# Kernel optimization log

Hardware: AMD Instinct MI355X
Metric: run time of the kernel (lower is better)

Reference implementation:

```python
import jax, jax.numpy as jnp
import numpy as np
from jax import lax

B = 16384  # batch; original torch module runs unbatched (1,5,27), we vectorize over B


def _conv(x, w, b, ph):
    # NCHW conv with kernel (kh,1), padding (ph,0), stride 1
    y = lax.conv_general_dilated(x, w, (1, 1), [(ph, ph), (0, 0)],
                                 dimension_numbers=('NCHW', 'OIHW', 'NCHW'))
    return y + b[None, :, None, None]


def _sl(x, w, b):
    # Semi_Linear: shared Linear applied over every (channel, height) slice ->
    # algebraically a single batched matmul on the last axis. w: (out,in)
    return jnp.einsum('bchw,ow->bcho', x, w) + b


def setup_inputs() -> dict:
    key = jax.random.key(0)
    ks = iter(jax.random.split(key, 40))
    def p(shape):
        return jax.random.normal(next(ks), shape, jnp.float32) * 0.05
    d = dict(
        x=jax.random.normal(next(ks), (B, 1, 5, 27), jnp.float32),
        w0a=p((5, 1, 3, 1)), b0a=p((5,)),
        wl0=p((18, 27)), bl0=p((18,)),
        w0b=p((25, 5, 3, 1)), b0b=p((25,)),
        w0c=p((25, 1, 1, 1)), b0c=p((25,)),
        wr0=p((18, 27)), br0=p((18,)),
        w1=p((75, 25, 2, 1)), b1=p((75,)),
        wl1=p((10, 18)), bl1=p((10,)),
        w2=p((125, 75, 2, 1)), b2=p((125,)),
        wa=p((125, 25, 3, 1)), ba=p((125,)),
        wra=p((10, 18)), bra=p((10,)),
        w0=p((300, 125, 2, 1)), b0=p((300,)),
        wl2=p((5, 10)), bl2=p((5,)),
        w0b2=p((512, 300, 2, 1)), b0b2=p((512,)),
        w0c2=p((512, 125, 3, 1)), b0c2=p((512,)),
        wr02=p((5, 10)), br02=p((5,)),
    )
    return d


def reference(x, w0a, b0a, wl0, bl0, w0b, b0b, w0c, b0c, wr0, br0,
              w1, b1, wl1, bl1, w2, b2, wa, ba, wra, bra,
              w0, b0, wl2, bl2, w0b2, b0b2, w0c2, b0c2, wr02, br02):
    # stage 0
    z = _conv(x, w0a, b0a, 1)                      # (B,5,5,27)
    z = jax.nn.relu(_sl(z, wl0, bl0))              # (B,5,5,18)
    z = _conv(z, w0b, b0b, 1)                      # (B,25,5,18)
    y = _conv(_sl(x, wr0, br0), w0c, b0c, 0)       # (B,25,5,18)
    x1 = z + y
    # stage 1
    z = _conv(x1, w1, b1, 0)                       # (B,75,4,18)
    z = jax.nn.relu(_sl(z, wl1, bl1))              # (B,75,4,10)
    z = _conv(z, w2, b2, 0)                        # (B,125,3,10)
    y = _conv(_sl(x1, wra, bra), wa, ba, 0)        # (B,125,3,10)
    x2 = z + y
    # stage 2
    z = _conv(x2, w0, b0, 0)                       # (B,300,2,10)
    z = jax.nn.relu(_sl(z, wl2, bl2))              # (B,300,2,5)
    z = _conv(z, w0b2, b0b2, 0)                    # (B,512,1,5)
    y = _conv(_sl(x2, wr02, br02), w0c2, b0c2, 0)  # (B,512,1,5)
    return z + y
```

## Files before the change

kernel.cpp:

```cpp
#include <hip/hip_runtime.h>
#include <stdint.h>


#define WB2T_OFF 0
#define WC2T_OFF 307200
#define W0T_OFF  499200
#define W1T_OFF  574200
#define WAT_OFF  577950
#define W2T_OFF  587325
#define WT_TOTAL 606075

__global__ __launch_bounds__(256)
void transpose_w(const float* __restrict__ w1, const float* __restrict__ wa,
                 const float* __restrict__ w2, const float* __restrict__ w0,
                 const float* __restrict__ wb2, const float* __restrict__ wc2,
                 float* __restrict__ ws) {
  int i = blockIdx.x * 256 + threadIdx.x;
  if (i < 3750) {
    int co = i / 50, k = i % 50;
    ws[W1T_OFF + k*75 + co] = w1[i];
  } else if (i < 13125) {
    int j = i - 3750; int co = j / 75, k = j % 75;
    ws[WAT_OFF + k*125 + co] = wa[j];
  } else if (i < 31875) {
    int j = i - 13125; int co = j / 150, k = j % 150;
    ws[W2T_OFF + k*125 + co] = w2[j];
  } else if (i < 106875) {
    int j = i - 31875; int co = j / 250, k = j % 250;
    ws[W0T_OFF + k*300 + co] = w0[j];
  } else if (i < 414075) {
    int j = i - 106875; int co = j / 600, k = j % 600;
    ws[WB2T_OFF + k*512 + co] = wb2[j];
  } else if (i < 606075) {
    int j = i - 414075; int co = j / 375, k = j % 375;
    ws[WC2T_OFF + k*512 + co] = wc2[j];
  }
}

template<int N>
__device__ __forceinline__ void ldrow(float* r, const float* p) {
  #pragma unroll
  for (int i = 0; i < N/4; ++i) {
    float4 q = reinterpret_cast<const float4*>(p)[i];
    r[4*i+0] = q.x; r[4*i+1] = q.y; r[4*i+2] = q.z; r[4*i+3] = q.w;
  }
}
template<int N>
__device__ __forceinline__ void strow(float* p, const float* r) {
  #pragma unroll
  for (int i = 0; i < N/4; ++i) {
    float4 q; q.x = r[4*i+0]; q.y = r[4*i+1]; q.z = r[4*i+2]; q.w = r[4*i+3];
    reinterpret_cast<float4*>(p)[i] = q;
  }
}

#define POOL   10112
#define X1_O   0
#define SX_O   2500
#define Z0A_O  2640
#define Z0SL_O 4500
#define T90_O  5000
#define Z1S_O  4500
#define T2_O   8100
#define X2_O   0
#define T3_O   4500
#define Z2S_O  6500

__global__ __launch_bounds__(256, 2)
void fused_net(const float* __restrict__ xg,
  const float* __restrict__ w0a_, const float* __restrict__ b0a_,
  const float* __restrict__ wl0_, const float* __restrict__ bl0_,
  const float* __restrict__ w0b_, const float* __restrict__ b0b_,
  const float* __restrict__ w0c_, const float* __restrict__ b0c_,
  const float* __restrict__ wr0_, const float* __restrict__ br0_,
  const float* __restrict__ b1_,
  const float* __restrict__ wl1_, const float* __restrict__ bl1_,
  const float* __restrict__ b2_,
  const float* __restrict__ ba_,
  const float* __restrict__ wra_, const float* __restrict__ bra_,
  const float* __restrict__ b0_,
  const float* __restrict__ wl2_, const float* __restrict__ bl2_,
  const float* __restrict__ b0b2_,
  const float* __restrict__ b0c2_,
  const float* __restrict__ wr02_,const float* __restrict__ br02_,
  const float* __restrict__ w1t, const float* __restrict__ wat,
  const float* __restrict__ w2t, const float* __restrict__ w0t,
  const float* __restrict__ wb2t, const float* __restrict__ wc2t,
  float* __restrict__ outg, int Btot)
{
  __shared__ __align__(16) float S[2*POOL];
  const int tid = threadIdx.x;
  const int b0 = blockIdx.x * 2;

  for (int i = tid; i < 270; i += 256) {
    int samp = i / 135, j = i % 135;
    int h = j / 27, w = j % 27;
    float v = 0.f;
    if (b0 + samp < Btot) v = xg[(size_t)(b0 + samp) * 135 + j];
    S[samp*POOL + SX_O + h*28 + w] = v;
  }
  __syncthreads();

  if (tid < 50) {
    int samp = tid / 25, r = tid % 25, co = r / 5, h = r % 5;
    float* P = S + samp*POOL;
    float acc[28];
    float bias = b0a_[co];
    #pragma unroll
    for (int w = 0; w < 28; ++w) acc[w] = bias;
    #pragma unroll
    for (int dh = 0; dh < 3; ++dh) {
      int hi = h + dh - 1;
      if (hi >= 0 && hi < 5) {
        float wf = w0a_[co*3 + dh];
        float row[28]; ldrow<28>(row, P + SX_O + hi*28);
        #pragma unroll
        for (int w = 0; w < 27; ++w) acc[w] += row[w] * wf;
      }
    }
    strow<28>(P + Z0A_O + (co*5 + h)*28, acc);
  }
  __syncthreads();

  if (tid < 180) {
    int samp = tid / 90, r = tid % 90;
    float* P = S + samp*POOL;
    if (r < 75) {
      int c = r / 15, q = r % 15, h = q / 3, o0 = (q % 3) * 6;
      float row[28]; ldrow<28>(row, P + Z0A_O + (c*5 + h)*28);
      float acc[6];
      #pragma unroll
      for (int k = 0; k < 6; ++k) acc[k] = bl0_[o0 + k];
      for (int w = 0; w < 27; ++w) {
        float rv = row[w];
        #pragma unroll
        for (int k = 0; k < 6; ++k) acc[k] += rv * wl0_[(o0 + k)*27 + w];
      }
      float* dst = P + Z0SL_O + (c*5 + h)*20 + o0;
      #pragma unroll
      for (int k = 0; k < 6; ++k) dst[k] = fmaxf(acc[k], 0.f);
    } else {
      int q = r - 75, h = q / 3, o0 = (q % 3) * 6;
      float row[28]; ldrow<28>(row, P + SX_O + h*28);
      float acc[6];
      #pragma unroll
      for (int k = 0; k < 6; ++k) acc[k] = br0_[o0 + k];
      for (int w = 0; w < 27; ++w) {
        float rv = row[w];
        #pragma unroll
        for (int k = 0; k < 6; ++k) acc[k] += rv * wr0_[(o0 + k)*27 + w];
      }
      float* dst = P + T90_O + h*20 + o0;
      #pragma unroll
      for (int k = 0; k < 6; ++k) dst[k] = acc[k];
    }
  }
  __syncthreads();

  if (tid < 250) {
    int samp = tid / 125, r = tid % 125, co = r / 5, h = r % 5;
    float* P = S + samp*POOL;
    float tr[20]; ldrow<20>(tr, P + T90_O + h*20);
    float wc = w0c_[co];
    float base = b0b_[co] + b0c_[co];
    float acc[20];
    #pragma unroll
    for (int o = 0; o < 18; ++o) acc[o] = base + tr[o]*wc;
    acc[18] = 0.f; acc[19] = 0.f;
    #pragma unroll
    for (int dh = 0; dh < 3; ++dh) {
      int hi = h + dh - 1;
      if (hi >= 0 && hi < 5) {
        #pragma unroll
        for (int ci = 0; ci < 5; ++ci) {
          float wgt = w0b_[(co*5 + ci)*3 + dh];
          float row[20]; ldrow<20>(row, P + Z0SL_O + (ci*5 + hi)*20);
          #pragma unroll
          for (int o = 0; o < 18; ++o) acc[o] += row[o] * wgt;
        }
      }
    }
    strow<20>(P + X1_O + (co*5 + h)*20, acc);
  }
  __syncthreads();

  for (int t = tid; t < 850; t += 256) {
    if (t < 600) {
      int samp = t / 300, r = t % 300, co = r / 4, h = r % 4;
      float* P = S + samp*POOL;
      float z1[18];
      float bias = b1_[co];
      #pragma unroll
      for (int w = 0; w < 18; ++w) z1[w] = bias;
      for (int ci = 0; ci < 25; ++ci) {
        float wx = w1t[(ci*2 + 0)*75 + co];
        float wy = w1t[(ci*2 + 1)*75 + co];
        float r0[20], r1[20];
        ldrow<20>(r0, P + X1_O + (ci*5 + h    )*20);
        ldrow<20>(r1, P + X1_O + (ci*5 + h + 1)*20);
        #pragma unroll
        for (int w = 0; w < 18; ++w) z1[w] += r0[w]*wx + r1[w]*wy;
      }
      float out[12];
      #pragma unroll
      for (int o = 0; o < 10; ++o) {
        float acc = bl1_[o];
        #pragma unroll
        for (int w = 0; w < 18; ++w) acc += z1[w] * wl1_[o*18 + w];
        out[o] = fmaxf(acc, 0.f);
      }
      out[10] = 0.f; out[11] = 0.f;
      strow<12>(P + Z1S_O + (co*4 + h)*12, out);
    } else {
      int q = t - 600;
      int samp = q / 125, r = q % 125, c = r / 5, h = r % 5;
      float* P = S + samp*POOL;
      float row[20]; ldrow<20>(row, P + X1_O + (c*5 + h)*20);
      float out[12];
      #pragma unroll
      for (int o = 0; o < 10; ++o) {
        float acc = bra_[o];
        #pragma unroll
        for (int w = 0; w < 18; ++w) acc += row[w] * wra_[o*18 + w];
        out[o] = acc;
      }
      out[10] = 0.f; out[11] = 0.f;
      strow<12>(P + T2_O + (c*5 + h)*12, out);
    }
  }
  __syncthreads();

  if (tid < 250) {
    int samp = tid / 125, co = tid % 125;
    float* P = S + samp*POOL;
    float acc[3][10];
    float bias = b2_[co] + ba_[co];
    #pragma unroll
    for (int h = 0; h < 3; ++h)
      #pragma unroll
      for (int w = 0; w < 10; ++w) acc[h][w] = bias;
    for (int ci = 0; ci < 25; ++ci) {
      float wf0 = wat[(ci*3 + 0)*125 + co];
      float wf1 = wat[(ci*3 + 1)*125 + co];
      float wf2 = wat[(ci*3 + 2)*125 + co];
      float rr[5][12];
      #pragma unroll
      for (int hh = 0; hh < 5; ++hh) ldrow<12>(rr[hh], P + T2_O + (ci*5 + hh)*12);
      #pragma unroll
      for (int h = 0; h < 3; ++h)
        #pragma unroll
        for (int w = 0; w < 10; ++w)
          acc[h][w] += rr[h][w]*wf0 + rr[h+1][w]*wf1 + rr[h+2][w]*wf2;
    }
    #pragma unroll
    for (int h = 0; h < 3; ++h) {
      float out[12];
      #pragma unroll
      for (int w = 0; w < 10; ++w) out[w] = acc[h][w];
      out[10] = 0.f; out[11] = 0.f;
      strow<12>(P + X2_O + (co*3 + h)*12, out);
    }
  }
  __syncthreads();

  if (tid < 250) {
    int samp = tid / 125, co = tid % 125;
    float* P = S + samp*POOL;
    float acc[3][12];
    #pragma unroll
    for (int h = 0; h < 3; ++h) ldrow<12>(acc[h], P + X2_O + (co*3 + h)*12);
    for (int ci = 0; ci < 75; ++ci) {
      float wx = w2t[(ci*2 + 0)*125 + co];
      float wy = w2t[(ci*2 + 1)*125 + co];
      float rr[4][12];
      #pragma unroll
      for (int hh = 0; hh < 4; ++hh) ldrow<12>(rr[hh], P + Z1S_O + (ci*4 + hh)*12);
      #pragma unroll
      for (int h = 0; h < 3; ++h)
        #pragma unroll
        for (int w = 0; w < 10; ++w)
          acc[h][w] += rr[h][w]*wx + rr[h+1][w]*wy;
    }
    #pragma unroll
    for (int h = 0; h < 3; ++h) strow<12>(P + X2_O + (co*3 + h)*12, acc[h]);
  }
  __syncthreads();

  for (int t = tid; t < 400; t += 256) {
    if (t < 150) {
      int samp = t / 75, cot = t % 75;
      int co = cot * 4;
      float* P = S + samp*POOL;
      float acc[4][2][10];
      #pragma unroll
      for (int j = 0; j < 4; ++j) {
        float bb = b0_[co + j];
        #pragma unroll
        for (int h = 0; h < 2; ++h)
          #pragma unroll
          for (int w = 0; w < 10; ++w) acc[j][h][w] = bb;
      }
      for (int ci = 0; ci < 125; ++ci) {
        float a0[12], a1[12], a2[12];
        ldrow<12>(a0, P + X2_O + (ci*3 + 0)*12);
        ldrow<12>(a1, P + X2_O + (ci*3 + 1)*12);
        ldrow<12>(a2, P + X2_O + (ci*3 + 2)*12);
        float4 wxv = *reinterpret_cast<const float4*>(w0t + (ci*2 + 0)*300 + co);
        float4 wyv = *reinterpret_cast<const float4*>(w0t + (ci*2 + 1)*300 + co);
        float wx[4] = {wxv.x, wxv.y, wxv.z, wxv.w};
        float wy[4] = {wyv.x, wyv.y, wyv.z, wyv.w};
        #pragma unroll
        for (int j = 0; j < 4; ++j)
          #pragma unroll
          for (int w = 0; w < 10; ++w) {
            acc[j][0][w] += a0[w]*wx[j] + a1[w]*wy[j];
            acc[j][1][w] += a1[w]*wx[j] + a2[w]*wy[j];
          }
      }
      #pragma unroll
      for (int j = 0; j < 4; ++j) {
        float out[12];
        #pragma unroll
        for (int h = 0; h < 2; ++h)
          #pragma unroll
          for (int o = 0; o < 5; ++o) {
            float sacc = bl2_[o];
            #pragma unroll
            for (int w = 0; w < 10; ++w) sacc += acc[j][h][w] * wl2_[o*10 + w];
            out[h*5 + o] = fmaxf(sacc, 0.f);
          }
        out[10] = 0.f; out[11] = 0.f;
        strow<12>(P + Z2S_O + (co + j)*12, out);
      }
    } else {
      int q = t - 150;
      int samp = q / 125, c = q % 125;
      float* P = S + samp*POOL;
      float rr[3][12];
      #pragma unroll
      for (int h = 0; h < 3; ++h) ldrow<12>(rr[h], P + X2_O + (c*3 + h)*12);
      float out[16];
      #pragma unroll
      for (int h = 0; h < 3; ++h)
        #pragma unroll
        for (int o = 0; o < 5; ++o) {
          float acc = br02_[o];
          #pragma unroll
          for (int w = 0; w < 10; ++w) acc += rr[h][w] * wr02_[o*10 + w];
          out[h*5 + o] = acc;
        }
      out[15] = 0.f;
      strow<16>(P + T3_O + c*16, out);
    }
  }
  __syncthreads();

  {
    int samp = tid >> 7, coq = tid & 127;
    int co = coq * 4;
    float* P = S + samp*POOL;
    float acc[4][5];
    #pragma unroll
    for (int j = 0; j < 4; ++j) {
      float bb = b0b2_[co + j] + b0c2_[co + j];
      #pragma unroll
      for (int w = 0; w < 5; ++w) acc[j][w] = bb;
    }
    for (int ci = 0; ci < 300; ++ci) {
      float a[12]; ldrow<12>(a, P + Z2S_O + ci*12);
      float4 uxv = *reinterpret_cast<const float4*>(wb2t + (ci*2 + 0)*512 + co);
      float4 uyv = *reinterpret_cast<const float4*>(wb2t + (ci*2 + 1)*512 + co);
      float ux[4] = {uxv.x, uxv.y, uxv.z, uxv.w};
      float uy[4] = {uyv.x, uyv.y, uyv.z, uyv.w};
      #pragma unroll
      for (int j = 0; j < 4; ++j)
        #pragma unroll
        for (int w = 0; w < 5; ++w)
          acc[j][w] += a[w]*ux[j] + a[5 + w]*uy[j];
    }
    for (int ci = 0; ci < 125; ++ci) {
      float t3[16]; ldrow<16>(t3, P + T3_O + ci*16);
      float4 u0v = *reinterpret_cast<const float4*>(wc2t + (ci*3 + 0)*512 + co);
      float4 u1v = *reinterpret_cast<const float4*>(wc2t + (ci*3 + 1)*512 + co);
      float4 u2v = *reinterpret_cast<const float4*>(wc2t + (ci*3 + 2)*512 + co);
      float u0[4] = {u0v.x, u0v.y, u0v.z, u0v.w};
      float u1[4] = {u1v.x, u1v.y, u1v.z, u1v.w};
      float u2[4] = {u2v.x, u2v.y, u2v.z, u2v.w};
      #pragma unroll
      for (int j = 0; j < 4; ++j)
        #pragma unroll
        for (int w = 0; w < 5; ++w)
          acc[j][w] += t3[w]*u0[j] + t3[5 + w]*u1[j] + t3[10 + w]*u2[j];
    }
    if (b0 + samp < Btot) {
      float* ob = outg + (size_t)(b0 + samp) * 2560 + co*5;
      float flat[20];
      #pragma unroll
      for (int j = 0; j < 4; ++j)
        #pragma unroll
        for (int w = 0; w < 5; ++w) flat[j*5 + w] = acc[j][w];
      strow<20>(ob, flat);
    }
  }
}

extern "C" void kernel_launch(void* const* d_in, const int* in_sizes, int n_in,
                              void* d_out, int out_size, void* d_ws, size_t ws_size,
                              hipStream_t stream) {
  (void)in_sizes; (void)n_in; (void)ws_size;
  const float* p[31];
  for (int i = 0; i < 31; ++i) p[i] = (const float*)d_in[i];
  float* ws = (float*)d_ws;

  transpose_w<<<(WT_TOTAL + 255) / 256, 256, 0, stream>>>(
      p[11] , p[17] , p[15] , p[21] ,
      p[25] , p[27] , ws);

  int Btot = out_size / 2560;
  int nb = (Btot + 1) >> 1;
  if (nb <= 0) return;
  fused_net<<<nb, 256, 0, stream>>>(
      p[0],
      p[1],  p[2],  p[3],  p[4],  p[5],  p[6],  p[7],  p[8],  p[9],  p[10],
      p[12],
      p[13], p[14],
      p[16],
      p[18],
      p[19], p[20],
      p[22],
      p[23], p[24],
      p[26],
      p[28],
      p[29], p[30],
      ws + W1T_OFF, ws + WAT_OFF, ws + W2T_OFF, ws + W0T_OFF,
      ws + WB2T_OFF, ws + WC2T_OFF,
      (float*)d_out, Btot);
}
```

Before: 3.461 ms.

## Double block size to 512 threads and split stage work finer per thread

Raises the fused kernel to 512 threads per block and redistributes the stage-1 convolutions so that each thread computes one output row instead of three. The final 512-channel stage now gives each thread two output channels instead of four. The aim is more active lanes in stages that previously left many threads idle. In exchange, the per-thread reuse of loaded rows and weights drops, so shared-memory and weight loads are repeated more, and register limits at 512 threads with two blocks per CU may constrain occupancy.

```diff
diff --git a/kernel.cpp b/kernel.cpp
--- a/kernel.cpp
+++ b/kernel.cpp
@@ -66,7 +66,9 @@
 #define T3_O   4500
 #define Z2S_O  6500
 
-__global__ __launch_bounds__(256, 2)
+#define NT 512
+
+__global__ __launch_bounds__(512, 2)
 void fused_net(const float* __restrict__ xg,
   const float* __restrict__ w0a_, const float* __restrict__ b0a_,
   const float* __restrict__ wl0_, const float* __restrict__ bl0_,
@@ -92,7 +94,7 @@
   const int tid = threadIdx.x;
   const int b0 = blockIdx.x * 2;
 
-  for (int i = tid; i < 270; i += 256) {
+  for (int i = tid; i < 270; i += NT) {
     int samp = i / 135, j = i % 135;
     int h = j / 27, w = j % 27;
     float v = 0.f;
@@ -184,7 +186,7 @@
   }
   __syncthreads();
 
-  for (int t = tid; t < 850; t += 256) {
+  for (int t = tid; t < 850; t += NT) {
     if (t < 600) {
       int samp = t / 300, r = t % 300, co = r / 4, h = r % 4;
       float* P = S + samp*POOL;
@@ -230,63 +232,54 @@
   }
   __syncthreads();
 
-  if (tid < 250) {
-    int samp = tid / 125, co = tid % 125;
-    float* P = S + samp*POOL;
-    float acc[3][10];
+  for (int t = tid; t < 750; t += NT) {
+    int samp = t / 375, r = t % 375, h = r / 125, co = r % 125;
+    float* P = S + samp*POOL;
+    float acc[10];
     float bias = b2_[co] + ba_[co];
     #pragma unroll
-    for (int h = 0; h < 3; ++h)
-      #pragma unroll
-      for (int w = 0; w < 10; ++w) acc[h][w] = bias;
+    for (int w = 0; w < 10; ++w) acc[w] = bias;
     for (int ci = 0; ci < 25; ++ci) {
       float wf0 = wat[(ci*3 + 0)*125 + co];
       float wf1 = wat[(ci*3 + 1)*125 + co];
       float wf2 = wat[(ci*3 + 2)*125 + co];
-      float rr[5][12];
-      #pragma unroll
-      for (int hh = 0; hh < 5; ++hh) ldrow<12>(rr[hh], P + T2_O + (ci*5 + hh)*12);
-      #pragma unroll
-      for (int h = 0; h < 3; ++h)
-        #pragma unroll
-        for (int w = 0; w < 10; ++w)
-          acc[h][w] += rr[h][w]*wf0 + rr[h+1][w]*wf1 + rr[h+2][w]*wf2;
-    }
-    #pragma unroll
-    for (int h = 0; h < 3; ++h) {
-      float out[12];
-      #pragma unroll
-      for (int w = 0; w < 10; ++w) out[w] = acc[h][w];
-      out[10] = 0.f; out[11] = 0.f;
-      strow<12>(P + X2_O + (co*3 + h)*12, out);
-    }
-  }
-  __syncthreads();
-
-  if (tid < 250) {
-    int samp = tid / 125, co = tid % 125;
-    float* P = S + samp*POOL;
-    float acc[3][12];
-    #pragma unroll
-    for (int h = 0; h < 3; ++h) ldrow<12>(acc[h], P + X2_O + (co*3 + h)*12);
+      float r0[12], r1[12], r2[12];
+      ldrow<12>(r0, P + T2_O + (ci*5 + h    )*12);
+      ldrow<12>(r1, P + T2_O + (ci*5 + h + 1)*12);
+      ldrow<12>(r2, P + T2_O + (ci*5 + h + 2)*12);
+      #pragma unroll
+      for (int w = 0; w < 10; ++w)
+        acc[w] += r0[w]*wf0 + r1[w]*wf1 + r2[w]*wf2;
+    }
+    float out[12];
+    #pragma unroll
+    for (int w = 0; w < 10; ++w) out[w] = acc[w];
+    out[10] = 0.f; out[11] = 0.f;
+    strow<12>(P + X2_O + (co*3 + h)*12, out);
+  }
+  __syncthreads();
+
+  for (int t = tid; t < 750; t += NT) {
+    int samp = t / 375, r = t % 375, h = r / 125, co = r % 125;
+    float* P = S + samp*POOL;
+    float acc[12];
+    ldrow<12>(acc, P + X2_O + (co*3 + h)*12);
     for (int ci = 0; ci < 75; ++ci) {
       float wx = w2t[(ci*2 + 0)*125 + co];
       float wy = w2t[(ci*2 + 1)*125 + co];
-      float rr[4][12];
-      #pragma unroll
-      for (int hh = 0; hh < 4; ++hh) ldrow<12>(rr[hh], P + Z1S_O + (ci*4 + hh)*12);
-      #pragma unroll
-      for (int h = 0; h < 3; ++h)
-        #pragma unroll
-        for (int w = 0; w < 10; ++w)
-          acc[h][w] += rr[h][w]*wx + rr[h+1][w]*wy;
-    }
-    #pragma unroll
-    for (int h = 0; h < 3; ++h) strow<12>(P + X2_O + (co*3 + h)*12, acc[h]);
-  }
-  __syncthreads();
-
-  for (int t = tid; t < 400; t += 256) {
+      float r0[12], r1[12];
+      ldrow<12>(r0, P + Z1S_O + (ci*4 + h    )*12);
+      ldrow<12>(r1, P + Z1S_O + (ci*4 + h + 1)*12);
+      #pragma unroll
+      for (int w = 0; w < 10; ++w)
+        acc[w] += r0[w]*wx + r1[w]*wy;
+    }
+    strow<12>(P + X2_O + (co*3 + h)*12, acc);
+  }
+  __syncthreads();
+
+  {
+    int t = tid;
     if (t < 150) {
       int samp = t / 75, cot = t % 75;
       int co = cot * 4;
@@ -332,7 +325,7 @@
         out[10] = 0.f; out[11] = 0.f;
         strow<12>(P + Z2S_O + (co + j)*12, out);
       }
-    } else {
+    } else if (t < 400) {
       int q = t - 150;
       int samp = q / 125, c = q % 125;
       float* P = S + samp*POOL;
@@ -356,50 +349,51 @@
   __syncthreads();
 
   {
-    int samp = tid >> 7, coq = tid & 127;
-    int co = coq * 4;
-    float* P = S + samp*POOL;
-    float acc[4][5];
-    #pragma unroll
-    for (int j = 0; j < 4; ++j) {
-      float bb = b0b2_[co + j] + b0c2_[co + j];
+    int samp = tid >> 8, pi = tid & 255;
+    int co0 = pi * 2;
+    float* P = S + samp*POOL;
+    float acc[2][5];
+    #pragma unroll
+    for (int j = 0; j < 2; ++j) {
+      float bb = b0b2_[co0 + j] + b0c2_[co0 + j];
       #pragma unroll
       for (int w = 0; w < 5; ++w) acc[j][w] = bb;
     }
     for (int ci = 0; ci < 300; ++ci) {
       float a[12]; ldrow<12>(a, P + Z2S_O + ci*12);
-      float4 uxv = *reinterpret_cast<const float4*>(wb2t + (ci*2 + 0)*512 + co);
-      float4 uyv = *reinterpret_cast<const float4*>(wb2t + (ci*2 + 1)*512 + co);
-      float ux[4] = {uxv.x, uxv.y, uxv.z, uxv.w};
-      float uy[4] = {uyv.x, uyv.y, uyv.z, uyv.w};
-      #pragma unroll
-      for (int j = 0; j < 4; ++j)
-        #pragma unroll
-        for (int w = 0; w < 5; ++w)
-          acc[j][w] += a[w]*ux[j] + a[5 + w]*uy[j];
+      float2 ux = *reinterpret_cast<const float2*>(wb2t + (ci*2 + 0)*512 + co0);
+      float2 uy = *reinterpret_cast<const float2*>(wb2t + (ci*2 + 1)*512 + co0);
+      #pragma unroll
+      for (int w = 0; w < 5; ++w) {
+        float p0 = a[w], p1 = a[5 + w];
+        acc[0][w] += p0*ux.x + p1*uy.x;
+        acc[1][w] += p0*ux.y + p1*uy.y;
+      }
     }
     for (int ci = 0; ci < 125; ++ci) {
       float t3[16]; ldrow<16>(t3, P + T3_O + ci*16);
-      float4 u0v = *reinterpret_cast<const float4*>(wc2t + (ci*3 + 0)*512 + co);
-      float4 u1v = *reinterpret_cast<const float4*>(wc2t + (ci*3 + 1)*512 + co);
-      float4 u2v = *reinterpret_cast<const float4*>(wc2t + (ci*3 + 2)*512 + co);
-      float u0[4] = {u0v.x, u0v.y, u0v.z, u0v.w};
-      float u1[4] = {u1v.x, u1v.y, u1v.z, u1v.w};
-      float u2[4] = {u2v.x, u2v.y, u2v.z, u2v.w};
-      #pragma unroll
-      for (int j = 0; j < 4; ++j)
-        #pragma unroll
-        for (int w = 0; w < 5; ++w)
-          acc[j][w] += t3[w]*u0[j] + t3[5 + w]*u1[j] + t3[10 + w]*u2[j];
+      float2 u0 = *reinterpret_cast<const float2*>(wc2t + (ci*3 + 0)*512 + co0);
+      float2 u1 = *reinterpret_cast<const float2*>(wc2t + (ci*3 + 1)*512 + co0);
+      float2 u2 = *reinterpret_cast<const float2*>(wc2t + (ci*3 + 2)*512 + co0);
+      #pragma unroll
+      for (int w = 0; w < 5; ++w) {
+        float p0 = t3[w], p1 = t3[5 + w], p2 = t3[10 + w];
+        acc[0][w] += p0*u0.x + p1*u1.x + p2*u2.x;
+        acc[1][w] += p0*u0.y + p1*u1.y + p2*u2.y;
+      }
     }
     if (b0 + samp < Btot) {
-      float* ob = outg + (size_t)(b0 + samp) * 2560 + co*5;
-      float flat[20];
-      #pragma unroll
-      for (int j = 0; j < 4; ++j)
+      float* ob = outg + (size_t)(b0 + samp) * 2560 + co0*5;
+      float flat[10];
+      #pragma unroll
+      for (int j = 0; j < 2; ++j)
         #pragma unroll
         for (int w = 0; w < 5; ++w) flat[j*5 + w] = acc[j][w];
-      strow<20>(ob, flat);
+      #pragma unroll
+      for (int k = 0; k < 5; ++k) {
+        float2 q; q.x = flat[2*k]; q.y = flat[2*k+1];
+        reinterpret_cast<float2*>(ob)[k] = q;
+      }
     }
   }
 }
@@ -419,7 +413,7 @@
   int Btot = out_size / 2560;
   int nb = (Btot + 1) >> 1;
   if (nb <= 0) return;
-  fused_net<<<nb, 256, 0, stream>>>(
+  fused_net<<<nb, NT, 0, stream>>>(
       p[0],
       p[1],  p[2],  p[3],  p[4],  p[5],  p[6],  p[7],  p[8],  p[9],  p[10],
       p[12],
```

After: 6.494 ms. 1.88x slower.

## Process samples sequentially per block with rotated thread mapping and fused stage-1 convs

Applied to the files above, without the earlier changes.

Each block now handles its two samples one after another with a single-sample shared pool instead of both at once. This halves LDS and allows raising launch bounds to three blocks per CU. Thread-to-work mapping is rotated per sample and block to spread active lanes across wavefronts. The two stage-1 output convolutions are merged into one accumulation pass, and the stage-2 conv uses two output channels per thread. The tradeoff is that many stages keep only a fraction of the block busy per sample, with more barriers per sample.

```diff
diff --git a/kernel.cpp b/kernel.cpp
--- a/kernel.cpp
+++ b/kernel.cpp
@@ -66,7 +66,7 @@
 #define T3_O   4500
 #define Z2S_O  6500
 
-__global__ __launch_bounds__(256, 2)
+__global__ __launch_bounds__(256, 3)
 void fused_net(const float* __restrict__ xg,
   const float* __restrict__ w0a_, const float* __restrict__ b0a_,
   const float* __restrict__ wl0_, const float* __restrict__ bl0_,
@@ -88,212 +88,194 @@
   const float* __restrict__ wb2t, const float* __restrict__ wc2t,
   float* __restrict__ outg, int Btot)
 {
-  __shared__ __align__(16) float S[2*POOL];
+  __shared__ __align__(16) float P[POOL];
   const int tid = threadIdx.x;
-  const int b0 = blockIdx.x * 2;
-
-  for (int i = tid; i < 270; i += 256) {
-    int samp = i / 135, j = i % 135;
-    int h = j / 27, w = j % 27;
-    float v = 0.f;
-    if (b0 + samp < Btot) v = xg[(size_t)(b0 + samp) * 135 + j];
-    S[samp*POOL + SX_O + h*28 + w] = v;
-  }
-  __syncthreads();
-
-  if (tid < 50) {
-    int samp = tid / 25, r = tid % 25, co = r / 5, h = r % 5;
-    float* P = S + samp*POOL;
-    float acc[28];
-    float bias = b0a_[co];
-    #pragma unroll
-    for (int w = 0; w < 28; ++w) acc[w] = bias;
-    #pragma unroll
-    for (int dh = 0; dh < 3; ++dh) {
-      int hi = h + dh - 1;
-      if (hi >= 0 && hi < 5) {
-        float wf = w0a_[co*3 + dh];
-        float row[28]; ldrow<28>(row, P + SX_O + hi*28);
-        #pragma unroll
-        for (int w = 0; w < 27; ++w) acc[w] += row[w] * wf;
-      }
-    }
-    strow<28>(P + Z0A_O + (co*5 + h)*28, acc);
-  }
-  __syncthreads();
-
-  if (tid < 180) {
-    int samp = tid / 90, r = tid % 90;
-    float* P = S + samp*POOL;
-    if (r < 75) {
-      int c = r / 15, q = r % 15, h = q / 3, o0 = (q % 3) * 6;
-      float row[28]; ldrow<28>(row, P + Z0A_O + (c*5 + h)*28);
-      float acc[6];
-      #pragma unroll
-      for (int k = 0; k < 6; ++k) acc[k] = bl0_[o0 + k];
-      for (int w = 0; w < 27; ++w) {
-        float rv = row[w];
-        #pragma unroll
-        for (int k = 0; k < 6; ++k) acc[k] += rv * wl0_[(o0 + k)*27 + w];
-      }
-      float* dst = P + Z0SL_O + (c*5 + h)*20 + o0;
-      #pragma unroll
-      for (int k = 0; k < 6; ++k) dst[k] = fmaxf(acc[k], 0.f);
-    } else {
-      int q = r - 75, h = q / 3, o0 = (q % 3) * 6;
-      float row[28]; ldrow<28>(row, P + SX_O + h*28);
-      float acc[6];
-      #pragma unroll
-      for (int k = 0; k < 6; ++k) acc[k] = br0_[o0 + k];
-      for (int w = 0; w < 27; ++w) {
-        float rv = row[w];
-        #pragma unroll
-        for (int k = 0; k < 6; ++k) acc[k] += rv * wr0_[(o0 + k)*27 + w];
-      }
-      float* dst = P + T90_O + h*20 + o0;
-      #pragma unroll
-      for (int k = 0; k < 6; ++k) dst[k] = acc[k];
-    }
-  }
-  __syncthreads();
-
-  if (tid < 250) {
-    int samp = tid / 125, r = tid % 125, co = r / 5, h = r % 5;
-    float* P = S + samp*POOL;
-    float tr[20]; ldrow<20>(tr, P + T90_O + h*20);
-    float wc = w0c_[co];
-    float base = b0b_[co] + b0c_[co];
-    float acc[20];
-    #pragma unroll
-    for (int o = 0; o < 18; ++o) acc[o] = base + tr[o]*wc;
-    acc[18] = 0.f; acc[19] = 0.f;
-    #pragma unroll
-    for (int dh = 0; dh < 3; ++dh) {
-      int hi = h + dh - 1;
-      if (hi >= 0 && hi < 5) {
-        #pragma unroll
-        for (int ci = 0; ci < 5; ++ci) {
-          float wgt = w0b_[(co*5 + ci)*3 + dh];
-          float row[20]; ldrow<20>(row, P + Z0SL_O + (ci*5 + hi)*20);
-          #pragma unroll
-          for (int o = 0; o < 18; ++o) acc[o] += row[o] * wgt;
-        }
-      }
-    }
-    strow<20>(P + X1_O + (co*5 + h)*20, acc);
-  }
-  __syncthreads();
-
-  for (int t = tid; t < 850; t += 256) {
-    if (t < 600) {
-      int samp = t / 300, r = t % 300, co = r / 4, h = r % 4;
-      float* P = S + samp*POOL;
-      float z1[18];
-      float bias = b1_[co];
-      #pragma unroll
-      for (int w = 0; w < 18; ++w) z1[w] = bias;
+
+  #pragma unroll 1
+  for (int si = 0; si < 2; ++si) {
+    const int b = blockIdx.x * 2 + si;
+    if (b >= Btot) break;
+    const int rot = ((blockIdx.x + si) & 3) << 6;
+    const int q = (tid + 256 - rot) & 255;
+
+    if (q < 135) {
+      int h = q / 27, w = q % 27;
+      P[SX_O + h*28 + w] = xg[(size_t)b * 135 + q];
+    }
+    __syncthreads();
+
+    if (q < 25) {
+      int co = q / 5, h = q % 5;
+      float acc[28];
+      float bias = b0a_[co];
+      #pragma unroll
+      for (int w = 0; w < 28; ++w) acc[w] = bias;
+      #pragma unroll
+      for (int dh = 0; dh < 3; ++dh) {
+        int hi = h + dh - 1;
+        if (hi >= 0 && hi < 5) {
+          float wf = w0a_[co*3 + dh];
+          float row[28]; ldrow<28>(row, P + SX_O + hi*28);
+          #pragma unroll
+          for (int w = 0; w < 27; ++w) acc[w] += row[w] * wf;
+        }
+      }
+      strow<28>(P + Z0A_O + (co*5 + h)*28, acc);
+    }
+    __syncthreads();
+
+    if (q < 90) {
+      if (q < 75) {
+        int c = q / 15, r = q % 15, h = r / 3, o0 = (r % 3) * 6;
+        float row[28]; ldrow<28>(row, P + Z0A_O + (c*5 + h)*28);
+        float acc[6];
+        #pragma unroll
+        for (int k = 0; k < 6; ++k) acc[k] = bl0_[o0 + k];
+        for (int w = 0; w < 27; ++w) {
+          float rv = row[w];
+          #pragma unroll
+          for (int k = 0; k < 6; ++k) acc[k] += rv * wl0_[(o0 + k)*27 + w];
+        }
+        float* dst = P + Z0SL_O + (c*5 + h)*20 + o0;
+        #pragma unroll
+        for (int k = 0; k < 6; ++k) dst[k] = fmaxf(acc[k], 0.f);
+      } else {
+        int r = q - 75, h = r / 3, o0 = (r % 3) * 6;
+        float row[28]; ldrow<28>(row, P + SX_O + h*28);
+        float acc[6];
+        #pragma unroll
+        for (int k = 0; k < 6; ++k) acc[k] = br0_[o0 + k];
+        for (int w = 0; w < 27; ++w) {
+          float rv = row[w];
+          #pragma unroll
+          for (int k = 0; k < 6; ++k) acc[k] += rv * wr0_[(o0 + k)*27 + w];
+        }
+        float* dst = P + T90_O + h*20 + o0;
+        #pragma unroll
+        for (int k = 0; k < 6; ++k) dst[k] = acc[k];
+      }
+    }
+    __syncthreads();
+
+    if (q < 125) {
+      int h = q / 25, co = q % 25;
+      float tr[20]; ldrow<20>(tr, P + T90_O + h*20);
+      float wc = w0c_[co];
+      float base = b0b_[co] + b0c_[co];
+      float acc[20];
+      #pragma unroll
+      for (int o = 0; o < 18; ++o) acc[o] = base + tr[o]*wc;
+      acc[18] = 0.f; acc[19] = 0.f;
+      #pragma unroll
+      for (int dh = 0; dh < 3; ++dh) {
+        int hi = h + dh - 1;
+        if (hi >= 0 && hi < 5) {
+          #pragma unroll
+          for (int ci = 0; ci < 5; ++ci) {
+            float wgt = w0b_[(co*5 + ci)*3 + dh];
+            float row[20]; ldrow<20>(row, P + Z0SL_O + (ci*5 + hi)*20);
+            #pragma unroll
+            for (int o = 0; o < 18; ++o) acc[o] += row[o] * wgt;
+          }
+        }
+      }
+      strow<20>(P + X1_O + (co*5 + h)*20, acc);
+    }
+    __syncthreads();
+
+    for (int t = q; t < 425; t += 256) {
+      if (t < 300) {
+        int h = t / 75, co = t % 75;
+        float z1[18];
+        float bias = b1_[co];
+        #pragma unroll
+        for (int w = 0; w < 18; ++w) z1[w] = bias;
+        for (int ci = 0; ci < 25; ++ci) {
+          float wx = w1t[(ci*2 + 0)*75 + co];
+          float wy = w1t[(ci*2 + 1)*75 + co];
+          float r0[20], r1[20];
+          ldrow<20>(r0, P + X1_O + (ci*5 + h    )*20);
+          ldrow<20>(r1, P + X1_O + (ci*5 + h + 1)*20);
+          #pragma unroll
+          for (int w = 0; w < 18; ++w) z1[w] += r0[w]*wx + r1[w]*wy;
+        }
+        float out[12];
+        #pragma unroll
+        for (int o = 0; o < 10; ++o) {
+          float acc = bl1_[o];
+          #pragma unroll
+          for (int w = 0; w < 18; ++w) acc += z1[w] * wl1_[o*18 + w];
+          out[o] = fmaxf(acc, 0.f);
+        }
+        out[10] = 0.f; out[11] = 0.f;
+        strow<12>(P + Z1S_O + (co*4 + h)*12, out);
+      } else {
+        int r = t - 300;
+        int h = r / 25, c = r % 25;
+        float row[20]; ldrow<20>(row, P + X1_O + (c*5 + h)*20);
+        float out[12];
+        #pragma unroll
+        for (int o = 0; o < 10; ++o) {
+          float acc = bra_[o];
+          #pragma unroll
+          for (int w = 0; w < 18; ++w) acc += row[w] * wra_[o*18 + w];
+          out[o] = acc;
+        }
+        out[10] = 0.f; out[11] = 0.f;
+        strow<12>(P + T2_O + (c*5 + h)*12, out);
+      }
+    }
+    __syncthreads();
+
+    if (q < 125) {
+      int co = q;
+      float acc[3][10];
+      float bias = b2_[co] + ba_[co];
+      #pragma unroll
+      for (int h = 0; h < 3; ++h)
+        #pragma unroll
+        for (int w = 0; w < 10; ++w) acc[h][w] = bias;
       for (int ci = 0; ci < 25; ++ci) {
-        float wx = w1t[(ci*2 + 0)*75 + co];
-        float wy = w1t[(ci*2 + 1)*75 + co];
-        float r0[20], r1[20];
-        ldrow<20>(r0, P + X1_O + (ci*5 + h    )*20);
-        ldrow<20>(r1, P + X1_O + (ci*5 + h + 1)*20);
-        #pragma unroll
-        for (int w = 0; w < 18; ++w) z1[w] += r0[w]*wx + r1[w]*wy;
-      }
-      float out[12];
-      #pragma unroll
-      for (int o = 0; o < 10; ++o) {
-        float acc = bl1_[o];
-        #pragma unroll
-        for (int w = 0; w < 18; ++w) acc += z1[w] * wl1_[o*18 + w];
-        out[o] = fmaxf(acc, 0.f);
-      }
-      out[10] = 0.f; out[11] = 0.f;
-      strow<12>(P + Z1S_O + (co*4 + h)*12, out);
-    } else {
-      int q = t - 600;
-      int samp = q / 125, r = q % 125, c = r / 5, h = r % 5;
-      float* P = S + samp*POOL;
-      float row[20]; ldrow<20>(row, P + X1_O + (c*5 + h)*20);
-      float out[12];
-      #pragma unroll
-      for (int o = 0; o < 10; ++o) {
-        float acc = bra_[o];
-        #pragma unroll
-        for (int w = 0; w < 18; ++w) acc += row[w] * wra_[o*18 + w];
-        out[o] = acc;
-      }
-      out[10] = 0.f; out[11] = 0.f;
-      strow<12>(P + T2_O + (c*5 + h)*12, out);
-    }
-  }
-  __syncthreads();
-
-  if (tid < 250) {
-    int samp = tid / 125, co = tid % 125;
-    float* P = S + samp*POOL;
-    float acc[3][10];
-    float bias = b2_[co] + ba_[co];
-    #pragma unroll
-    for (int h = 0; h < 3; ++h)
-      #pragma unroll
-      for (int w = 0; w < 10; ++w) acc[h][w] = bias;
-    for (int ci = 0; ci < 25; ++ci) {
-      float wf0 = wat[(ci*3 + 0)*125 + co];
-      float wf1 = wat[(ci*3 + 1)*125 + co];
-      float wf2 = wat[(ci*3 + 2)*125 + co];
-      float rr[5][12];
-      #pragma unroll
-      for (int hh = 0; hh < 5; ++hh) ldrow<12>(rr[hh], P + T2_O + (ci*5 + hh)*12);
-      #pragma unroll
-      for (int h = 0; h < 3; ++h)
-        #pragma unroll
-        for (int w = 0; w < 10; ++w)
-          acc[h][w] += rr[h][w]*wf0 + rr[h+1][w]*wf1 + rr[h+2][w]*wf2;
-    }
-    #pragma unroll
-    for (int h = 0; h < 3; ++h) {
-      float out[12];
-      #pragma unroll
-      for (int w = 0; w < 10; ++w) out[w] = acc[h][w];
-      out[10] = 0.f; out[11] = 0.f;
-      strow<12>(P + X2_O + (co*3 + h)*12, out);
-    }
-  }
-  __syncthreads();
-
-  if (tid < 250) {
-    int samp = tid / 125, co = tid % 125;
-    float* P = S + samp*POOL;
-    float acc[3][12];
-    #pragma unroll
-    for (int h = 0; h < 3; ++h) ldrow<12>(acc[h], P + X2_O + (co*3 + h)*12);
-    for (int ci = 0; ci < 75; ++ci) {
-      float wx = w2t[(ci*2 + 0)*125 + co];
-      float wy = w2t[(ci*2 + 1)*125 + co];
-      float rr[4][12];
-      #pragma unroll
-      for (int hh = 0; hh < 4; ++hh) ldrow<12>(rr[hh], P + Z1S_O + (ci*4 + hh)*12);
-      #pragma unroll
-      for (int h = 0; h < 3; ++h)
-        #pragma unroll
-        for (int w = 0; w < 10; ++w)
-          acc[h][w] += rr[h][w]*wx + rr[h+1][w]*wy;
-    }
-    #pragma unroll
-    for (int h = 0; h < 3; ++h) strow<12>(P + X2_O + (co*3 + h)*12, acc[h]);
-  }
-  __syncthreads();
-
-  for (int t = tid; t < 400; t += 256) {
-    if (t < 150) {
-      int samp = t / 75, cot = t % 75;
-      int co = cot * 4;
-      float* P = S + samp*POOL;
-      float acc[4][2][10];
-      #pragma unroll
-      for (int j = 0; j < 4; ++j) {
+        float wf0 = wat[(ci*3 + 0)*125 + co];
+        float wf1 = wat[(ci*3 + 1)*125 + co];
+        float wf2 = wat[(ci*3 + 2)*125 + co];
+        float rr[5][12];
+        #pragma unroll
+        for (int hh = 0; hh < 5; ++hh) ldrow<12>(rr[hh], P + T2_O + (ci*5 + hh)*12);
+        #pragma unroll
+        for (int h = 0; h < 3; ++h)
+          #pragma unroll
+          for (int w = 0; w < 10; ++w)
+            acc[h][w] += rr[h][w]*wf0 + rr[h+1][w]*wf1 + rr[h+2][w]*wf2;
+      }
+      for (int ci = 0; ci < 75; ++ci) {
+        float wx = w2t[(ci*2 + 0)*125 + co];
+        float wy = w2t[(ci*2 + 1)*125 + co];
+        float rr[4][12];
+        #pragma unroll
+        for (int hh = 0; hh < 4; ++hh) ldrow<12>(rr[hh], P + Z1S_O + (ci*4 + hh)*12);
+        #pragma unroll
+        for (int h = 0; h < 3; ++h)
+          #pragma unroll
+          for (int w = 0; w < 10; ++w)
+            acc[h][w] += rr[h][w]*wx + rr[h+1][w]*wy;
+      }
+      #pragma unroll
+      for (int h = 0; h < 3; ++h) {
+        float out[12];
+        #pragma unroll
+        for (int w = 0; w < 10; ++w) out[w] = acc[h][w];
+        out[10] = 0.f; out[11] = 0.f;
+        strow<12>(P + X2_O + (co*3 + h)*12, out);
+      }
+    }
+    __syncthreads();
+
+    if (q < 150) {
+      int co = q * 2;
+      float acc[2][2][10];
+      #pragma unroll
+      for (int j = 0; j < 2; ++j) {
         float bb = b0_[co + j];
         #pragma unroll
         for (int h = 0; h < 2; ++h)
@@ -305,12 +287,12 @@
         ldrow<12>(a0, P + X2_O + (ci*3 + 0)*12);
         ldrow<12>(a1, P + X2_O + (ci*3 + 1)*12);
         ldrow<12>(a2, P + X2_O + (ci*3 + 2)*12);
-        float4 wxv = *reinterpret_cast<const float4*>(w0t + (ci*2 + 0)*300 + co);
-        float4 wyv = *reinterpret_cast<const float4*>(w0t + (ci*2 + 1)*300 + co);
-        float wx[4] = {wxv.x, wxv.y, wxv.z, wxv.w};
-        float wy[4] = {wyv.x, wyv.y, wyv.z, wyv.w};
-        #pragma unroll
-        for (int j = 0; j < 4; ++j)
+        float2 wxv = *reinterpret_cast<const float2*>(w0t + (ci*2 + 0)*300 + co);
+        float2 wyv = *reinterpret_cast<const float2*>(w0t + (ci*2 + 1)*300 + co);
+        float wx[2] = {wxv.x, wxv.y};
+        float wy[2] = {wyv.x, wyv.y};
+        #pragma unroll
+        for (int j = 0; j < 2; ++j)
           #pragma unroll
           for (int w = 0; w < 10; ++w) {
             acc[j][0][w] += a0[w]*wx[j] + a1[w]*wy[j];
@@ -318,7 +300,7 @@
           }
       }
       #pragma unroll
-      for (int j = 0; j < 4; ++j) {
+      for (int j = 0; j < 2; ++j) {
         float out[12];
         #pragma unroll
         for (int h = 0; h < 2; ++h)
@@ -332,68 +314,68 @@
         out[10] = 0.f; out[11] = 0.f;
         strow<12>(P + Z2S_O + (co + j)*12, out);
       }
-    } else {
-      int q = t - 150;
-      int samp = q / 125, c = q % 125;
-      float* P = S + samp*POOL;
-      float rr[3][12];
-      #pragma unroll
-      for (int h = 0; h < 3; ++h) ldrow<12>(rr[h], P + X2_O + (c*3 + h)*12);
-      float out[16];
-      #pragma unroll
-      for (int h = 0; h < 3; ++h)
-        #pragma unroll
-        for (int o = 0; o < 5; ++o) {
-          float acc = br02_[o];
-          #pragma unroll
-          for (int w = 0; w < 10; ++w) acc += rr[h][w] * wr02_[o*10 + w];
-          out[h*5 + o] = acc;
-        }
-      out[15] = 0.f;
-      strow<16>(P + T3_O + c*16, out);
-    }
-  }
-  __syncthreads();
-
-  {
-    int samp = tid >> 7, coq = tid & 127;
-    int co = coq * 4;
-    float* P = S + samp*POOL;
-    float acc[4][5];
-    #pragma unroll
-    for (int j = 0; j < 4; ++j) {
-      float bb = b0b2_[co + j] + b0c2_[co + j];
-      #pragma unroll
-      for (int w = 0; w < 5; ++w) acc[j][w] = bb;
-    }
-    for (int ci = 0; ci < 300; ++ci) {
-      float a[12]; ldrow<12>(a, P + Z2S_O + ci*12);
-      float4 uxv = *reinterpret_cast<const float4*>(wb2t + (ci*2 + 0)*512 + co);
-      float4 uyv = *reinterpret_cast<const float4*>(wb2t + (ci*2 + 1)*512 + co);
-      float ux[4] = {uxv.x, uxv.y, uxv.z, uxv.w};
-      float uy[4] = {uyv.x, uyv.y, uyv.z, uyv.w};
-      #pragma unroll
-      for (int j = 0; j < 4; ++j)
-        #pragma unroll
-        for (int w = 0; w < 5; ++w)
-          acc[j][w] += a[w]*ux[j] + a[5 + w]*uy[j];
-    }
-    for (int ci = 0; ci < 125; ++ci) {
-      float t3[16]; ldrow<16>(t3, P + T3_O + ci*16);
-      float4 u0v = *reinterpret_cast<const float4*>(wc2t + (ci*3 + 0)*512 + co);
-      float4 u1v = *reinterpret_cast<const float4*>(wc2t + (ci*3 + 1)*512 + co);
-      float4 u2v = *reinterpret_cast<const float4*>(wc2t + (ci*3 + 2)*512 + co);
-      float u0[4] = {u0v.x, u0v.y, u0v.z, u0v.w};
-      float u1[4] = {u1v.x, u1v.y, u1v.z, u1v.w};
-      float u2[4] = {u2v.x, u2v.y, u2v.z, u2v.w};
-      #pragma unroll
-      for (int j = 0; j < 4; ++j)
-        #pragma unroll
-        for (int w = 0; w < 5; ++w)
-          acc[j][w] += t3[w]*u0[j] + t3[5 + w]*u1[j] + t3[10 + w]*u2[j];
-    }
-    if (b0 + samp < Btot) {
-      float* ob = outg + (size_t)(b0 + samp) * 2560 + co*5;
+    } else if (q < 213) {
+      int r = q - 150;
+      #pragma unroll
+      for (int cc = 0; cc < 2; ++cc) {
+        int c = r*2 + cc;
+        if (c < 125) {
+          float rr[3][12];
+          #pragma unroll
+          for (int h = 0; h < 3; ++h) ldrow<12>(rr[h], P + X2_O + (c*3 + h)*12);
+          float out[16];
+          #pragma unroll
+          for (int h = 0; h < 3; ++h)
+            #pragma unroll
+            for (int o = 0; o < 5; ++o) {
+              float acc = br02_[o];
+              #pragma unroll
+              for (int w = 0; w < 10; ++w) acc += rr[h][w] * wr02_[o*10 + w];
+              out[h*5 + o] = acc;
+            }
+          out[15] = 0.f;
+          strow<16>(P + T3_O + c*16, out);
+        }
+      }
+    }
+    __syncthreads();
+
+    if (q < 128) {
+      int co = q * 4;
+      float acc[4][5];
+      #pragma unroll
+      for (int j = 0; j < 4; ++j) {
+        float bb = b0b2_[co + j] + b0c2_[co + j];
+        #pragma unroll
+        for (int w = 0; w < 5; ++w) acc[j][w] = bb;
+      }
+      for (int ci = 0; ci < 300; ++ci) {
+        float a[12]; ldrow<12>(a, P + Z2S_O + ci*12);
+        float4 uxv = *reinterpret_cast<const float4*>(wb2t + (ci*2 + 0)*512 + co);
+        float4 uyv = *reinterpret_cast<const float4*>(wb2t + (ci*2 + 1)*512 + co);
+        float ux[4] = {uxv.x, uxv.y, uxv.z, uxv.w};
+        float uy[4] = {uyv.x, uyv.y, uyv.z, uyv.w};
+        #pragma unroll
+        for (int j = 0; j < 4; ++j)
+          #pragma unroll
+          for (int w = 0; w < 5; ++w)
+            acc[j][w] += a[w]*ux[j] + a[5 + w]*uy[j];
+      }
+      for (int ci = 0; ci < 125; ++ci) {
+        float t3[16]; ldrow<16>(t3, P + T3_O + ci*16);
+        float4 u0v = *reinterpret_cast<const float4*>(wc2t + (ci*3 + 0)*512 + co);
+        float4 u1v = *reinterpret_cast<const float4*>(wc2t + (ci*3 + 1)*512 + co);
+        float4 u2v = *reinterpret_cast<const float4*>(wc2t + (ci*3 + 2)*512 + co);
+        float u0[4] = {u0v.x, u0v.y, u0v.z, u0v.w};
+        float u1[4] = {u1v.x, u1v.y, u1v.z, u1v.w};
+        float u2[4] = {u2v.x, u2v.y, u2v.z, u2v.w};
+        #pragma unroll
+        for (int j = 0; j < 4; ++j)
+          #pragma unroll
+          for (int w = 0; w < 5; ++w)
+            acc[j][w] += t3[w]*u0[j] + t3[5 + w]*u1[j] + t3[10 + w]*u2[j];
+      }
+      float* ob = outg + (size_t)b * 2560 + co*5;
       float flat[20];
       #pragma unroll
       for (int j = 0; j < 4; ++j)
@@ -401,6 +383,7 @@
         for (int w = 0; w < 5; ++w) flat[j*5 + w] = acc[j][w];
       strow<20>(ob, flat);
     }
+    __syncthreads();
   }
 }
 
@@ -417,8 +400,8 @@
       p[25] , p[27] , ws);
 
   int Btot = out_size / 2560;
+  if (Btot <= 0) return;
   int nb = (Btot + 1) >> 1;
-  if (nb <= 0) return;
   fused_net<<<nb, 256, 0, stream>>>(
       p[0],
       p[1],  p[2],  p[3],  p[4],  p[5],  p[6],  p[7],  p[8],  p[9],  p[10],
```

New measurement: 4.452 ms. 28.6% more time.
